# Kernel optimization log

Measured on AMD Instinct MI355X. Metric: run time of the kernel, lower is better.

## Reference

```python
import jax, jax.numpy as jnp
import numpy as np
from math import gcd


def get_start_index(length):
    # phase offset used by the torch module when striding the full conv output
    return 0 if length <= 2 else (length - 1) // 2


def setup_inputs() -> dict:
    key = jax.random.key(0)
    k1, k2 = jax.random.split(key)
    N = 8388608      # input signal length
    FILT = 128       # FIR filter taps
    x = jax.random.normal(k1, (N,), dtype=jnp.float32)
    filter_coeffs = jax.random.normal(k2, (FILT,), dtype=jnp.float32)
    return {"x": x, "filter_coeffs": filter_coeffs, "up": 2, "down": 3}


def reference(x, filter_coeffs, up, down):
    # gcd-reduce the rational rate factor, as the torch forward does
    g = gcd(up, down)
    up, down = up // g, down // g
    if up == 1 and down == 1:
        return x
    N = x.shape[0]
    filt_size = filter_coeffs.shape[0]
    # 1) zero-insertion upsample, scaled by `up`  ->  length up*N
    x_up = jnp.zeros(up * N, dtype=x.dtype).at[::up].set(up * x)
    # 2) torch.conv1d with flipped filter and padding=filt_size-1 is a true
    #    'full' linear convolution  ->  length up*N + filt_size - 1
    full = jnp.convolve(x_up, filter_coeffs, mode='full')
    # 3) phase-offset strided downsample, 4) truncate to ceil(N*up/down)
    start = get_start_index(filt_size)
    total = N * up
    out_len = total // down + (1 if total % down else 0)
    return full[start::down][:out_len]
```

## Files before the change

kernel.cpp:

```cpp
#include <hip/hip_runtime.h>
#include <hip/hip_bf16.h>


typedef __bf16 bf16x8 __attribute__((ext_vector_type(8)));
typedef float  f32x4  __attribute__((ext_vector_type(4)));

constexpr int BT  = 256;
constexpr int GPB = 4096;
constexpr int XT  = 3 * GPB + 96;
constexpr int XT4 = XT / 4;

__global__ __launch_bounds__(BT) void resample23_mfma(
    const float* __restrict__ x,
    const float* __restrict__ filt,
    float* __restrict__ out,
    int N, int out_size)
{
    __shared__ __align__(16) unsigned short xs[XT];

    const int t = threadIdx.x;
    const int w = t >> 6;
    const int l = t & 63;
    const int G0 = blockIdx.x * GPB;
    const long F0 = 3L * G0 - 32;

    const bool interior = (F0 >= 0) && (F0 + XT <= (long)N);
    #pragma unroll
    for (int r = 0; r < (XT4 + BT - 1) / BT; ++r) {
        int idx = t + BT * r;
        if (idx < XT4) {
            long f0 = F0 + 4L * idx;
            float4 v;
            if (interior) {
                v = *reinterpret_cast<const float4*>(x + f0);
            } else {
                v.x = (f0 + 0 >= 0 && f0 + 0 < N) ? x[f0 + 0] : 0.0f;
                v.y = (f0 + 1 >= 0 && f0 + 1 < N) ? x[f0 + 1] : 0.0f;
                v.z = (f0 + 2 >= 0 && f0 + 2 < N) ? x[f0 + 2] : 0.0f;
                v.w = (f0 + 3 >= 0 && f0 + 3 < N) ? x[f0 + 3] : 0.0f;
            }
            __hip_bfloat162 p0 = __float22bfloat162_rn(make_float2(v.x, v.y));
            __hip_bfloat162 p1 = __float22bfloat162_rn(make_float2(v.z, v.w));
            *reinterpret_cast<__hip_bfloat162*>(&xs[4 * idx + 0]) = p0;
            *reinterpret_cast<__hip_bfloat162*>(&xs[4 * idx + 2]) = p1;
        }
    }

    const int j   = l & 15;
    const int kq  = (l >> 4) * 8;
    const int dlt = j >> 1;
    const int ph  = j & 1;
    bf16x8 Bf[3];
    #pragma unroll
    for (int kc = 0; kc < 3; ++kc) {
        #pragma unroll
        for (int e = 0; e < 8; ++e) {
            int k = 32 * kc + kq + e;
            int v = k - 3 * dlt - 2 * ph;
            float fv = (v >= 0 && v < 64) ? filt[(ph ? 126 : 127) - 2 * v] : 0.0f;
            Bf[kc][e] = (__bf16)fv;
        }
    }

    __syncthreads();

    const char* xsb = reinterpret_cast<const char*>(xs);
    #pragma unroll
    for (int s = 0; s < 8; ++s) {
        const int g0   = G0 + 128 * (8 * w + s);
        const int boff = 768 * (8 * w + s) + 48 * (l & 15) + 16 * (l >> 4);

        f32x4 acc = {0.0f, 0.0f, 0.0f, 0.0f};
        #pragma unroll
        for (int kc = 0; kc < 3; ++kc) {
            bf16x8 a = *reinterpret_cast<const bf16x8*>(xsb + boff + 64 * kc);
            acc = __builtin_amdgcn_mfma_f32_16x16x32_bf16(a, Bf[kc], acc, 0, 0, 0);
        }

        const int obase = 2 * g0 + 16 * (4 * (l >> 4)) + j;
        #pragma unroll
        for (int r = 0; r < 4; ++r) {
            int o = obase + 16 * r;
            if (o < out_size) out[o] = 2.0f * acc[r];
        }
    }
}

extern "C" void kernel_launch(void* const* d_in, const int* in_sizes, int n_in,
                              void* d_out, int out_size, void* d_ws, size_t ws_size,
                              hipStream_t stream)
{
    const float* x    = (const float*)d_in[0];
    const float* filt = (const float*)d_in[1];
    float* out        = (float*)d_out;
    const int N       = in_sizes[0];

    const int n_pairs = (out_size + 1) / 2;
    const int blocks  = (n_pairs + GPB - 1) / GPB;
    resample23_mfma<<<blocks, BT, 0, stream>>>(x, filt, out, N, out_size);
}
```

Measured before the change: 17.78 us.

## Precompute bf16 filter fragments in a setup kernel and shrink per-block work

Adds a small setup kernel that builds the per-lane bf16 MFMA B-fragments from the filter once and stores them in workspace. The main kernel then loads three vectors per lane instead of running 24 gather-and-convert steps per thread. The per-block tile drops from 4096 to 1024 output pairs, giving four times as many blocks with a smaller LDS tile, which should spread the memory-bound work across more CUs. In exchange it adds a second launch and more halo reloads between neighbouring blocks.

```diff
diff --git a/kernel.cpp b/kernel.cpp
--- a/kernel.cpp
+++ b/kernel.cpp
@@ -6,13 +6,30 @@
 typedef float  f32x4  __attribute__((ext_vector_type(4)));
 
 constexpr int BT  = 256;
-constexpr int GPB = 4096;
+constexpr int GPB = 1024;
+constexpr int UPW = GPB / 128 / 4;
 constexpr int XT  = 3 * GPB + 96;
 constexpr int XT4 = XT / 4;
 
+__global__ void build_btab(const float* __restrict__ filt,
+                           unsigned short* __restrict__ btab)
+{
+    const int l = threadIdx.x;
+    const int j = l & 15, kq = (l >> 4) * 8, dlt = j >> 1, ph = j & 1;
+    for (int kc = 0; kc < 3; ++kc) {
+        for (int e = 0; e < 8; ++e) {
+            int k = 32 * kc + kq + e;
+            int v = k - 3 * dlt - 2 * ph;
+            float fv = (v >= 0 && v < 64) ? filt[(ph ? 126 : 127) - 2 * v] : 0.0f;
+            __hip_bfloat16 b = __float2bfloat16(fv);
+            btab[(kc * 64 + l) * 8 + e] = *reinterpret_cast<unsigned short*>(&b);
+        }
+    }
+}
+
 __global__ __launch_bounds__(BT) void resample23_mfma(
     const float* __restrict__ x,
-    const float* __restrict__ filt,
+    const unsigned short* __restrict__ btab,
     float* __restrict__ out,
     int N, int out_size)
 {
@@ -21,8 +38,14 @@
     const int t = threadIdx.x;
     const int w = t >> 6;
     const int l = t & 63;
+    const int j = l & 15;
     const int G0 = blockIdx.x * GPB;
     const long F0 = 3L * G0 - 32;
+
+    const bf16x8* bt = reinterpret_cast<const bf16x8*>(btab);
+    bf16x8 Bf0 = bt[0 * 64 + l];
+    bf16x8 Bf1 = bt[1 * 64 + l];
+    bf16x8 Bf2 = bt[2 * 64 + l];
 
     const bool interior = (F0 >= 0) && (F0 + XT <= (long)N);
     #pragma unroll
@@ -45,39 +68,24 @@
             *reinterpret_cast<__hip_bfloat162*>(&xs[4 * idx + 2]) = p1;
         }
     }
-
-    const int j   = l & 15;
-    const int kq  = (l >> 4) * 8;
-    const int dlt = j >> 1;
-    const int ph  = j & 1;
-    bf16x8 Bf[3];
-    #pragma unroll
-    for (int kc = 0; kc < 3; ++kc) {
-        #pragma unroll
-        for (int e = 0; e < 8; ++e) {
-            int k = 32 * kc + kq + e;
-            int v = k - 3 * dlt - 2 * ph;
-            float fv = (v >= 0 && v < 64) ? filt[(ph ? 126 : 127) - 2 * v] : 0.0f;
-            Bf[kc][e] = (__bf16)fv;
-        }
-    }
-
     __syncthreads();
 
     const char* xsb = reinterpret_cast<const char*>(xs);
     #pragma unroll
-    for (int s = 0; s < 8; ++s) {
-        const int g0   = G0 + 128 * (8 * w + s);
-        const int boff = 768 * (8 * w + s) + 48 * (l & 15) + 16 * (l >> 4);
+    for (int s = 0; s < UPW; ++s) {
+        const int u    = UPW * w + s;
+        const int g0   = G0 + 128 * u;
+        const int boff = 768 * u + 48 * j + 16 * (l >> 4);
 
         f32x4 acc = {0.0f, 0.0f, 0.0f, 0.0f};
-        #pragma unroll
-        for (int kc = 0; kc < 3; ++kc) {
-            bf16x8 a = *reinterpret_cast<const bf16x8*>(xsb + boff + 64 * kc);
-            acc = __builtin_amdgcn_mfma_f32_16x16x32_bf16(a, Bf[kc], acc, 0, 0, 0);
-        }
+        bf16x8 a0 = *reinterpret_cast<const bf16x8*>(xsb + boff + 0);
+        bf16x8 a1 = *reinterpret_cast<const bf16x8*>(xsb + boff + 64);
+        bf16x8 a2 = *reinterpret_cast<const bf16x8*>(xsb + boff + 128);
+        acc = __builtin_amdgcn_mfma_f32_16x16x32_bf16(a0, Bf0, acc, 0, 0, 0);
+        acc = __builtin_amdgcn_mfma_f32_16x16x32_bf16(a1, Bf1, acc, 0, 0, 0);
+        acc = __builtin_amdgcn_mfma_f32_16x16x32_bf16(a2, Bf2, acc, 0, 0, 0);
 
-        const int obase = 2 * g0 + 16 * (4 * (l >> 4)) + j;
+        const int obase = 2 * g0 + 64 * (l >> 4) + j;
         #pragma unroll
         for (int r = 0; r < 4; ++r) {
             int o = obase + 16 * r;
@@ -94,8 +102,11 @@
     const float* filt = (const float*)d_in[1];
     float* out        = (float*)d_out;
     const int N       = in_sizes[0];
+    unsigned short* btab = (unsigned short*)d_ws;
+
+    build_btab<<<1, 64, 0, stream>>>(filt, btab);
 
     const int n_pairs = (out_size + 1) / 2;
     const int blocks  = (n_pairs + GPB - 1) / GPB;
-    resample23_mfma<<<blocks, BT, 0, stream>>>(x, filt, out, N, out_size);
+    resample23_mfma<<<blocks, BT, 0, stream>>>(x, btab, out, N, out_size);
 }
```

Result: slower. 20.47 us (+15.1%).

## Stream input via per-wave async global-to-LDS loads with double-buffered tiles

Applied to the files above, without the earlier changes.

Replaces the block-wide bf16 LDS staging and __syncthreads with per-wave fp32 tiles loaded directly into LDS through global_load_lds. Two buffers per wave let the next tile's load overlap with the MFMA compute on the current one. Conversion to bf16 moves to the point where MFMA operands are read. Each block now handles 4 tiles of 512 pairs instead of one 4096-pair tile. This avoids the staging pass through registers and the block barrier, at the cost of hand-placed waitcnt ordering, more LDS reads, and a smaller per-block grain.

```diff
diff --git a/kernel.cpp b/kernel.cpp
--- a/kernel.cpp
+++ b/kernel.cpp
@@ -5,51 +5,40 @@
 typedef __bf16 bf16x8 __attribute__((ext_vector_type(8)));
 typedef float  f32x4  __attribute__((ext_vector_type(4)));
 
-constexpr int BT  = 256;
-constexpr int GPB = 4096;
-constexpr int XT  = 3 * GPB + 96;
-constexpr int XT4 = XT / 4;
+constexpr int BT    = 256;
+constexpr int GPB   = 512;
+constexpr int TPB   = 4;
+constexpr int WSL   = 512;
+constexpr int XSPAN = 1664;
+
+__device__ __forceinline__ void gload_lds16(const float* g, float* l) {
+    __builtin_amdgcn_global_load_lds(
+        (const __attribute__((address_space(1))) void*)g,
+        (__attribute__((address_space(3))) void*)l, 16, 0, 0);
+}
+
+__device__ __forceinline__ bf16x8 cvt8(float4 a, float4 b) {
+    union { bf16x8 v; __hip_bfloat162 h[4]; } u;
+    u.h[0] = __float22bfloat162_rn(make_float2(a.x, a.y));
+    u.h[1] = __float22bfloat162_rn(make_float2(a.z, a.w));
+    u.h[2] = __float22bfloat162_rn(make_float2(b.x, b.y));
+    u.h[3] = __float22bfloat162_rn(make_float2(b.z, b.w));
+    return u.v;
+}
 
 __global__ __launch_bounds__(BT) void resample23_mfma(
     const float* __restrict__ x,
     const float* __restrict__ filt,
     float* __restrict__ out,
-    int N, int out_size)
+    int N, int out_size, int n_tiles)
 {
-    __shared__ __align__(16) unsigned short xs[XT];
+    __shared__ __align__(16) float xs[2][4][WSL];
 
     const int t = threadIdx.x;
-    const int w = t >> 6;
-    const int l = t & 63;
-    const int G0 = blockIdx.x * GPB;
-    const long F0 = 3L * G0 - 32;
+    const int w = t >> 6, l = t & 63;
+    const int j = l & 15, q = l >> 4;
 
-    const bool interior = (F0 >= 0) && (F0 + XT <= (long)N);
-    #pragma unroll
-    for (int r = 0; r < (XT4 + BT - 1) / BT; ++r) {
-        int idx = t + BT * r;
-        if (idx < XT4) {
-            long f0 = F0 + 4L * idx;
-            float4 v;
-            if (interior) {
-                v = *reinterpret_cast<const float4*>(x + f0);
-            } else {
-                v.x = (f0 + 0 >= 0 && f0 + 0 < N) ? x[f0 + 0] : 0.0f;
-                v.y = (f0 + 1 >= 0 && f0 + 1 < N) ? x[f0 + 1] : 0.0f;
-                v.z = (f0 + 2 >= 0 && f0 + 2 < N) ? x[f0 + 2] : 0.0f;
-                v.w = (f0 + 3 >= 0 && f0 + 3 < N) ? x[f0 + 3] : 0.0f;
-            }
-            __hip_bfloat162 p0 = __float22bfloat162_rn(make_float2(v.x, v.y));
-            __hip_bfloat162 p1 = __float22bfloat162_rn(make_float2(v.z, v.w));
-            *reinterpret_cast<__hip_bfloat162*>(&xs[4 * idx + 0]) = p0;
-            *reinterpret_cast<__hip_bfloat162*>(&xs[4 * idx + 2]) = p1;
-        }
-    }
-
-    const int j   = l & 15;
-    const int kq  = (l >> 4) * 8;
-    const int dlt = j >> 1;
-    const int ph  = j & 1;
+    const int kq = q * 8, dlt = j >> 1, ph = j & 1;
     bf16x8 Bf[3];
     #pragma unroll
     for (int kc = 0; kc < 3; ++kc) {
@@ -62,26 +51,63 @@
         }
     }
 
-    __syncthreads();
+    const int t0 = blockIdx.x * TPB;
+    const int te = (t0 + TPB < n_tiles) ? t0 + TPB : n_tiles;
+    const int rb = 24 * j + 8 * q;
 
-    const char* xsb = reinterpret_cast<const char*>(xs);
-    #pragma unroll
-    for (int s = 0; s < 8; ++s) {
-        const int g0   = G0 + 128 * (8 * w + s);
-        const int boff = 768 * (8 * w + s) + 48 * (l & 15) + 16 * (l >> 4);
-
+    auto compute = [&](int tt, const float* wavebuf) {
+        const float* bp = wavebuf + rb;
+        bf16x8 A0 = cvt8(*(const float4*)(bp +  0), *(const float4*)(bp +  4));
+        bf16x8 A1 = cvt8(*(const float4*)(bp + 32), *(const float4*)(bp + 36));
+        bf16x8 A2 = cvt8(*(const float4*)(bp + 64), *(const float4*)(bp + 68));
         f32x4 acc = {0.0f, 0.0f, 0.0f, 0.0f};
-        #pragma unroll
-        for (int kc = 0; kc < 3; ++kc) {
-            bf16x8 a = *reinterpret_cast<const bf16x8*>(xsb + boff + 64 * kc);
-            acc = __builtin_amdgcn_mfma_f32_16x16x32_bf16(a, Bf[kc], acc, 0, 0, 0);
-        }
-
-        const int obase = 2 * g0 + 16 * (4 * (l >> 4)) + j;
+        acc = __builtin_amdgcn_mfma_f32_16x16x32_bf16(A0, Bf[0], acc, 0, 0, 0);
+        acc = __builtin_amdgcn_mfma_f32_16x16x32_bf16(A1, Bf[1], acc, 0, 0, 0);
+        acc = __builtin_amdgcn_mfma_f32_16x16x32_bf16(A2, Bf[2], acc, 0, 0, 0);
+        const int obase = 2 * (tt * GPB + 128 * w) + 64 * q + j;
         #pragma unroll
         for (int r = 0; r < 4; ++r) {
             int o = obase + 16 * r;
             if (o < out_size) out[o] = 2.0f * acc[r];
+        }
+    };
+
+    auto stage_fast = [&](int tt, float* wavebuf) {
+        const float* src = x + (3L * tt * GPB - 32) + 384 * w + 4 * l;
+        float* dst = wavebuf + 4 * l;
+        gload_lds16(src, dst);
+        gload_lds16(src + 256, dst + 256);
+    };
+
+    const long lastF0 = 3L * (t0 + TPB - 1) * GPB - 32;
+    const bool fast = (t0 > 0) && (te == t0 + TPB) && (lastF0 + XSPAN <= (long)N);
+
+    if (fast) {
+        stage_fast(t0 + 0, xs[0][w]);
+        stage_fast(t0 + 1, xs[1][w]);
+        asm volatile("s_waitcnt vmcnt(2)" ::: "memory");
+        compute(t0 + 0, xs[0][w]);
+        asm volatile("s_waitcnt lgkmcnt(0)" ::: "memory");
+        stage_fast(t0 + 2, xs[0][w]);
+        asm volatile("s_waitcnt vmcnt(6)" ::: "memory");
+        compute(t0 + 1, xs[1][w]);
+        asm volatile("s_waitcnt lgkmcnt(0)" ::: "memory");
+        stage_fast(t0 + 3, xs[1][w]);
+        asm volatile("s_waitcnt vmcnt(6)" ::: "memory");
+        compute(t0 + 2, xs[0][w]);
+        asm volatile("s_waitcnt vmcnt(4)" ::: "memory");
+        compute(t0 + 3, xs[1][w]);
+    } else {
+        for (int tt = t0; tt < te; ++tt) {
+            float* wavebuf = xs[tt & 1][w];
+            const long F0 = 3L * tt * GPB - 32 + 384 * w;
+            #pragma unroll
+            for (int k = 0; k < 8; ++k) {
+                long gi = F0 + 64 * k + l;
+                wavebuf[64 * k + l] = (gi >= 0 && gi < (long)N) ? x[gi] : 0.0f;
+            }
+            __builtin_amdgcn_s_waitcnt(0);
+            compute(tt, wavebuf);
         }
     }
 }
@@ -96,6 +122,7 @@
     const int N       = in_sizes[0];
 
     const int n_pairs = (out_size + 1) / 2;
-    const int blocks  = (n_pairs + GPB - 1) / GPB;
-    resample23_mfma<<<blocks, BT, 0, stream>>>(x, filt, out, N, out_size);
+    const int n_tiles = (n_pairs + GPB - 1) / GPB;
+    const int blocks  = (n_tiles + TPB - 1) / TPB;
+    resample23_mfma<<<blocks, BT, 0, stream>>>(x, filt, out, N, out_size, n_tiles);
 }
```

After: 24.48 us. +37.7%, slower.
